# Performance work log

Hardware: AMD Instinct MI355X
Metric: run time of the kernel (lower is better)

## Reference

```python
import jax, jax.numpy as jnp
import numpy as np

N = 20000      # nodes
E = 160000     # edges (avg degree 16)
IN_DIM = 256
HID = 128      # hidden_dim == per-head out_channels in PyG TransformerConv
HEADS = 4
EPS = 1e-5


def setup_inputs() -> dict:
    key = jax.random.key(0)
    ks = jax.random.split(key, 24)

    def w(k, shape, scale=0.05):
        return jax.random.normal(k, shape, dtype=jnp.float32) * scale

    inp = {
        "x": jax.random.normal(ks[0], (N, IN_DIM), dtype=jnp.float32),
        "edge_index": jax.random.randint(ks[1], (2, E), 0, N, dtype=jnp.int32),
        # input projection
        "lin_w": w(ks[2], (IN_DIM, HID)), "lin_b": jnp.zeros((HID,), jnp.float32),
    }
    i = 3
    for l in (1, 2):
        inp[f"q_w{l}"] = w(ks[i], (HID, HEADS * HID)); i += 1
        inp[f"q_b{l}"] = jnp.zeros((HEADS * HID,), jnp.float32)
        inp[f"k_w{l}"] = w(ks[i], (HID, HEADS * HID)); i += 1
        inp[f"k_b{l}"] = jnp.zeros((HEADS * HID,), jnp.float32)
        inp[f"v_w{l}"] = w(ks[i], (HID, HEADS * HID)); i += 1
        inp[f"v_b{l}"] = jnp.zeros((HEADS * HID,), jnp.float32)
        inp[f"s_w{l}"] = w(ks[i], (HID, HID)); i += 1
        inp[f"s_b{l}"] = jnp.zeros((HID,), jnp.float32)
        inp[f"ln_g{l}"] = jnp.ones((HID,), jnp.float32)
        inp[f"ln_b{l}"] = jnp.zeros((HID,), jnp.float32)
    return inp


def _segment_softmax(scores, seg, num):
    # scores: [E, HEADS], seg: [E] destination indices
    m = jax.ops.segment_max(scores, seg, num_segments=num)
    m = jnp.where(jnp.isfinite(m), m, 0.0)  # guard empty segments
    e = jnp.exp(scores - m[seg])
    d = jax.ops.segment_sum(e, seg, num_segments=num)
    return e / (d[seg] + 1e-16)


def _transformer_conv(x, src, dst, qw, qb, kw, kb, vw, vb, sw, sb):
    # PyG TransformerConv(HID, HID, heads=HEADS, concat=False)
    n = x.shape[0]
    q = (x @ qw + qb).reshape(n, HEADS, HID)
    k = (x @ kw + kb).reshape(n, HEADS, HID)
    v = (x @ vw + vb).reshape(n, HEADS, HID)
    # per-edge attention: query at dst (i), key/value at src (j)
    alpha = jnp.einsum("ehd,ehd->eh", q[dst], k[src]) / jnp.sqrt(jnp.float32(HID))
    alpha = _segment_softmax(alpha, dst, n)                 # [E, HEADS]
    msg = v[src] * alpha[..., None]                          # [E, HEADS, HID]
    out = jax.ops.segment_sum(msg, dst, num_segments=n)      # [N, HEADS, HID]
    out = out.mean(axis=1)                                   # concat=False -> head mean
    return out + x @ sw + sb                                 # root skip connection


def _layer_norm(x, g, b):
    mu = x.mean(-1, keepdims=True)
    var = ((x - mu) ** 2).mean(-1, keepdims=True)
    return (x - mu) * jax.lax.rsqrt(var + EPS) * g + b


def reference(x, edge_index, lin_w, lin_b,
              q_w1, q_b1, k_w1, k_b1, v_w1, v_b1, s_w1, s_b1, ln_g1, ln_b1,
              q_w2, q_b2, k_w2, k_b2, v_w2, v_b2, s_w2, s_b2, ln_g2, ln_b2):
    src, dst = edge_index[0], edge_index[1]
    h = jax.nn.relu(x @ lin_w + lin_b)
    h1 = _transformer_conv(h, src, dst, q_w1, q_b1, k_w1, k_b1, v_w1, v_b1, s_w1, s_b1)
    h = _layer_norm(h1 + h, ln_g1, ln_b1)
    h2 = _transformer_conv(h, src, dst, q_w2, q_b2, k_w2, k_b2, v_w2, v_b2, s_w2, s_b2)
    h = _layer_norm(h2 + h, ln_g2, ln_b2)
    return h
```

## Files before the change

### kernel.cpp

```cpp
#include <hip/hip_runtime.h>
#include <math.h>

#define NNODE 20000
#define NEDGE 160000
#define IN_DIMV 256
#define HIDV 128
#define DEGCAP 64
#define BAT 4

typedef __attribute__((ext_vector_type(8))) short bf16x8;
typedef __attribute__((ext_vector_type(4))) float f32x4;
typedef __attribute__((ext_vector_type(2))) float f32x2;

__device__ __forceinline__ float bf2f(unsigned short u) {
    union { unsigned int i; float f; } x; x.i = ((unsigned int)u) << 16; return x.f;
}
__device__ __forceinline__ unsigned short f2bf(float f) {
    union { float f; unsigned int i; } x; x.f = f;
    unsigned int r = x.i + 0x7fffu + ((x.i >> 16) & 1u);
    return (unsigned short)(r >> 16);
}
__device__ __forceinline__ void unpack8(uint4 p, float* f) {
    f[0] = bf2f((unsigned short)(p.x & 0xffff)); f[1] = bf2f((unsigned short)(p.x >> 16));
    f[2] = bf2f((unsigned short)(p.y & 0xffff)); f[3] = bf2f((unsigned short)(p.y >> 16));
    f[4] = bf2f((unsigned short)(p.z & 0xffff)); f[5] = bf2f((unsigned short)(p.z >> 16));
    f[6] = bf2f((unsigned short)(p.w & 0xffff)); f[7] = bf2f((unsigned short)(p.w >> 16));
}
__device__ __forceinline__ void unpack8f8_w(unsigned int a, unsigned int b, float* f) {
    f32x2 t;
    t = __builtin_amdgcn_cvt_pk_f32_fp8((int)a, false); f[0] = t.x; f[1] = t.y;
    t = __builtin_amdgcn_cvt_pk_f32_fp8((int)a, true);  f[2] = t.x; f[3] = t.y;
    t = __builtin_amdgcn_cvt_pk_f32_fp8((int)b, false); f[4] = t.x; f[5] = t.y;
    t = __builtin_amdgcn_cvt_pk_f32_fp8((int)b, true);  f[6] = t.x; f[7] = t.y;
}
__device__ __forceinline__ unsigned char f2fp8(float v) {
    int pk = __builtin_amdgcn_cvt_pk_fp8_f32(v, v, 0, false);
    return (unsigned char)(pk & 0xff);
}
__device__ __forceinline__ void gld_lds16(const unsigned short* g, unsigned short* l) {
    __builtin_amdgcn_global_load_lds((const __attribute__((address_space(1))) void*)g,
                                     (__attribute__((address_space(3))) void*)l, 16, 0, 0);
}

__global__ void convert_kernel(
    const float* __restrict__ lin_w,
    const float* __restrict__ qw0, const float* __restrict__ kw0,
    const float* __restrict__ vw0, const float* __restrict__ sw0,
    const float* __restrict__ qw1, const float* __restrict__ kw1,
    const float* __restrict__ vw1, const float* __restrict__ sw1,
    unsigned short* __restrict__ arena, int* __restrict__ cursor)
{
    int idx = blockIdx.x * 256 + threadIdx.x;
    if (idx < NNODE) cursor[idx] = 0;
    int id2 = idx - NNODE;
    if (id2 < 0 || id2 >= 458752) return;
    float v;
    if (id2 < 32768) {
        int n = id2 >> 8, k = id2 & 255;
        v = lin_w[k * 128 + n];
    } else {
        int t = id2 - 32768;
        int l = t / 212992, r = t % 212992;
        int n = r >> 7, k = r & 127;
        const float* qw = l ? qw1 : qw0;
        const float* kw = l ? kw1 : kw0;
        const float* vw = l ? vw1 : vw0;
        const float* sw = l ? sw1 : sw0;
        if (n < 1536) {
            const float* w = (n < 512) ? qw : (n < 1024) ? kw : vw;
            v = w[k * 512 + (n & 511)];
        } else {
            v = sw[k * 128 + (n - 1536)];
        }
    }
    arena[id2] = f2bf(v);
}

__global__ __launch_bounds__(256) void mfma_gemm0(
    const float* __restrict__ A, const unsigned short* __restrict__ WT,
    const float* __restrict__ b0, unsigned short* __restrict__ hbf_out)
{
    __shared__ unsigned short smem[8192];
    unsigned short* As = smem;
    unsigned short* Bs = smem + 4096;
    unsigned short* ot = smem;
    const int K = 256;

    int tid = threadIdx.x;
    int lane = tid & 63;
    int w = tid >> 6;
    int wm = w & 1, wn = w >> 1;
    int bm = blockIdx.x * 128;

    int r0 = tid >> 2;
    int c0 = (tid & 3) * 8;
    int g0 = bm + r0;      if (g0 > NNODE - 1) g0 = NNODE - 1;
    int g1 = bm + r0 + 64; if (g1 > NNODE - 1) g1 = NNODE - 1;
    int srow = lane >> 2;
    int scol = (lane & 3) * 8;
    int br0 = w * 32 + srow;
    int br1 = w * 32 + 16 + srow;

    f32x4 acc[4][4] = {};
    int arow = wm * 64 + (lane & 15);
    int brow = wn * 64 + (lane & 15);
    int koff = (lane >> 4) * 8;

    for (int k0 = 0; k0 < K; k0 += 32) {
        {
            const float4* p0 = (const float4*)(A + (size_t)g0 * K + k0 + c0);
            float4 u = p0[0], v = p0[1];
            unsigned short t0[8] = {f2bf(u.x), f2bf(u.y), f2bf(u.z), f2bf(u.w),
                                    f2bf(v.x), f2bf(v.y), f2bf(v.z), f2bf(v.w)};
            *(uint4*)&As[r0 * 32 + c0] = *(uint4*)t0;
            const float4* p1 = (const float4*)(A + (size_t)g1 * K + k0 + c0);
            u = p1[0]; v = p1[1];
            unsigned short t1[8] = {f2bf(u.x), f2bf(u.y), f2bf(u.z), f2bf(u.w),
                                    f2bf(v.x), f2bf(v.y), f2bf(v.z), f2bf(v.w)};
            *(uint4*)&As[(r0 + 64) * 32 + c0] = *(uint4*)t1;
        }
        gld_lds16(WT + (size_t)br0 * K + k0 + scol, Bs + (w * 32) * 32);
        gld_lds16(WT + (size_t)br1 * K + k0 + scol, Bs + (w * 32 + 16) * 32);
        __syncthreads();
        bf16x8 fa[4], fb[4];
#pragma unroll
        for (int i = 0; i < 4; i++) fa[i] = *(const bf16x8*)&As[(arow + i * 16) * 32 + koff];
#pragma unroll
        for (int i = 0; i < 4; i++) fb[i] = *(const bf16x8*)&Bs[(brow + i * 16) * 32 + koff];
#pragma unroll
        for (int mi = 0; mi < 4; mi++)
#pragma unroll
            for (int ni = 0; ni < 4; ni++)
                acc[mi][ni] = __builtin_amdgcn_mfma_f32_16x16x32_bf16(fa[mi], fb[ni], acc[mi][ni], 0, 0, 0);
        __syncthreads();
    }

    int quad = lane >> 4, lcol = lane & 15;
#pragma unroll
    for (int hh = 0; hh < 2; hh++) {
        __syncthreads();
        if (wm == hh) {
#pragma unroll
            for (int mi = 0; mi < 4; mi++) {
#pragma unroll
                for (int ni = 0; ni < 4; ni++) {
                    int lc = wn * 64 + ni * 16 + lcol;
                    float bias = b0[lc];
#pragma unroll
                    for (int reg = 0; reg < 4; reg++) {
                        float v = fmaxf(acc[mi][ni][reg] + bias, 0.f);
                        ot[(mi * 16 + quad * 4 + reg) * 128 + lc] = f2bf(v);
                    }
                }
            }
        }
        __syncthreads();
        int r = tid >> 2, ch = tid & 3;
        int row = bm + hh * 64 + r;
        if (row < NNODE) {
            uint4* dp = (uint4*)(hbf_out + (size_t)row * HIDV + ch * 32);
            const uint4* sp = (const uint4*)(ot + r * 128 + ch * 32);
#pragma unroll
            for (int q = 0; q < 4; q++) dp[q] = sp[q];
        }
    }
}

__global__ __launch_bounds__(256) void mfma_gemm1(
    const unsigned short* __restrict__ A, const unsigned short* __restrict__ WT,
    const float* __restrict__ b0, const float* __restrict__ b1,
    const float* __restrict__ b2, const float* __restrict__ b3,
    unsigned short* __restrict__ qb_out, unsigned char* __restrict__ kv8_out,
    unsigned short* __restrict__ pre16_out)
{
    __shared__ unsigned short As[8192];
    __shared__ unsigned short Ws[16384];
    unsigned short* ot = Ws;
    unsigned char* ot8 = (unsigned char*)Ws;
    const int K = 128;

    int tid = threadIdx.x;
    int lane = tid & 63;
    int w = tid >> 6;
    int bm = blockIdx.x * 64;
    int p0 = (blockIdx.y == 0) ? 0 : 7;
    int p1 = (blockIdx.y == 0) ? 7 : 13;

    int srow = lane >> 2;
    int scol = (lane & 3) * 8;
    int asr = w * 16 + srow;
    int aar = bm + asr; if (aar > NNODE - 1) aar = NNODE - 1;
    int sr0 = w * 32 + srow;
    int sr1 = w * 32 + 16 + srow;

#pragma unroll
    for (int c = 0; c < 4; c++) {
        gld_lds16(A + (size_t)aar * K + c * 32 + scol, As + c * 2048 + asr * 32);
    }

    int arow = lane & 15;
    int koff = (lane >> 4) * 8;
    int quad = lane >> 4, lcol = lane & 15;

    for (int p = p0; p < p1; p++) {
        int bn = p * 128;
#pragma unroll
        for (int c = 0; c < 4; c++) {
            gld_lds16(WT + (size_t)(bn + sr0) * K + c * 32 + scol, Ws + c * 4096 + sr0 * 32);
            gld_lds16(WT + (size_t)(bn + sr1) * K + c * 32 + scol, Ws + c * 4096 + sr1 * 32);
        }
        __syncthreads();

        f32x4 acc[4][2] = {};
#pragma unroll
        for (int c = 0; c < 4; c++) {
            bf16x8 fa[4], fb[2];
#pragma unroll
            for (int i = 0; i < 4; i++) fa[i] = *(const bf16x8*)&As[c * 2048 + (arow + i * 16) * 32 + koff];
#pragma unroll
            for (int i = 0; i < 2; i++) fb[i] = *(const bf16x8*)&Ws[c * 4096 + (w * 32 + i * 16 + arow) * 32 + koff];
#pragma unroll
            for (int mi = 0; mi < 4; mi++)
#pragma unroll
                for (int ni = 0; ni < 2; ni++)
                    acc[mi][ni] = __builtin_amdgcn_mfma_f32_16x16x32_bf16(fa[mi], fb[ni], acc[mi][ni], 0, 0, 0);
        }
        __syncthreads();

        if (p < 4 || p == 12) {
            const float* bb = (p < 4) ? (b0 + bn) : b3;
#pragma unroll
            for (int mi = 0; mi < 4; mi++) {
#pragma unroll
                for (int ni = 0; ni < 2; ni++) {
                    int lc = w * 32 + ni * 16 + lcol;
                    float bias = bb[lc];
#pragma unroll
                    for (int reg = 0; reg < 4; reg++)
                        ot[(mi * 16 + quad * 4 + reg) * 128 + lc] = f2bf(acc[mi][ni][reg] + bias);
                }
            }
            __syncthreads();
            int r = tid >> 2, q = tid & 3;
            int row = bm + r;
            if (row < NNODE) {
                unsigned short* dst = (p < 4) ? (qb_out + (size_t)row * 512 + bn + q * 32)
                                              : (pre16_out + (size_t)row * HIDV + q * 32);
                const uint4* sp = (const uint4*)(ot + r * 128 + q * 32);
                uint4* dp = (uint4*)dst;
#pragma unroll
                for (int qq = 0; qq < 4; qq++) dp[qq] = sp[qq];
            }
            __syncthreads();
        } else {
            const float* bb = (bn < 1024) ? (b1 + bn - 512) : (b2 + bn - 1024);
            int coff = bn - 512;
#pragma unroll
            for (int mi = 0; mi < 4; mi++) {
#pragma unroll
                for (int ni = 0; ni < 2; ni++) {
                    int lc = w * 32 + ni * 16 + lcol;
                    float bias = bb[lc];
#pragma unroll
                    for (int reg = 0; reg < 4; reg++)
                        ot8[(mi * 16 + quad * 4 + reg) * 128 + lc] = f2fp8(acc[mi][ni][reg] + bias);
                }
            }
            __syncthreads();
            int r = tid >> 2, q = tid & 3;
            int row = bm + r;
            if (row < NNODE) {
                uint4* dp = (uint4*)(kv8_out + (size_t)row * 1024 + coff + q * 32);
                const uint4* sp = (const uint4*)(ot8 + r * 128 + q * 32);
                dp[0] = sp[0]; dp[1] = sp[1];
            }
            __syncthreads();
        }
    }
}

__global__ void scatter_kernel(const int* __restrict__ ei, int* __restrict__ cursor,
                               int* __restrict__ bucket) {
    int e = blockIdx.x * blockDim.x + threadIdx.x;
    if (e < NEDGE) {
        int d = ei[NEDGE + e];
        int slot = atomicAdd(&cursor[d], 1);
        if (slot < DEGCAP) bucket[d * DEGCAP + slot] = ei[e];
    }
}

__global__ __launch_bounds__(256) void attn_ln_kernel(
    const unsigned short* __restrict__ qb, const unsigned char* __restrict__ kv8,
    const int* __restrict__ cursor, const int* __restrict__ bucket,
    const unsigned short* __restrict__ pre16, const float* __restrict__ g,
    const float* __restrict__ b,
    unsigned short* __restrict__ hbf ,
    float* __restrict__ extout)
{
    int lane = threadIdx.x & 63;
    int wid = threadIdx.x >> 6;
    int i = blockIdx.x * 4 + wid;
    int myidx = bucket[i * DEGCAP + lane];
    int cnt = cursor[i]; if (cnt > DEGCAP) cnt = DEGCAP;

    int hg = lane >> 4;
    int sl = lane & 15;
    int off = hg * 128 + sl * 8;

    size_t base = (size_t)i * HIDV + sl * 8;
    uint4 pv_raw = *(const uint4*)(pre16 + base);
    uint4 hv_raw = *(const uint4*)(hbf + base);

    float qr[8];
    {
        uint4 p = *(const uint4*)(qb + (size_t)i * 512 + lane * 8);
        unpack8(p, qr);
#pragma unroll
        for (int j = 0; j < 8; j++) qr[j] *= 0.0883883476483184f;
    }

    float m = -INFINITY, l = 0.f;
    float acc[8] = {0.f, 0.f, 0.f, 0.f, 0.f, 0.f, 0.f, 0.f};

    if (cnt > 0) {
        uint2 kA[BAT], vA[BAT], kB[BAT], vB[BAT];

        auto issue = [&](uint2 (&KB)[BAT], uint2 (&VB)[BAT], int bb) {
#pragma unroll
            for (int t = 0; t < BAT; t++) {
                int j = bb * BAT + t; if (j >= cnt) j = cnt - 1;
                int src = __shfl(myidx, j);
                const unsigned char* bp = kv8 + (size_t)src * 1024 + off;
                KB[t] = *(const uint2*)bp;
                VB[t] = *(const uint2*)(bp + 512);
            }
        };

        auto consume = [&](const uint2 (&KB)[BAT], const uint2 (&VB)[BAT], int bb) {
            int rem = cnt - bb * BAT;
            float d[BAT];
#pragma unroll
            for (int t = 0; t < BAT; t++) d[t] = -3.0e38f;
#pragma unroll
            for (int t = 0; t < BAT; t++) {
                if (t >= rem) break;
                float kf[8];
                unpack8f8_w(KB[t].x, KB[t].y, kf);
                d[t] = qr[0] * kf[0] + qr[1] * kf[1] + qr[2] * kf[2] + qr[3] * kf[3] +
                       qr[4] * kf[4] + qr[5] * kf[5] + qr[6] * kf[6] + qr[7] * kf[7];
            }
#pragma unroll
            for (int t = 0; t < BAT; t++) { if (t >= rem) break; d[t] += __shfl_xor(d[t], 8); }
#pragma unroll
            for (int t = 0; t < BAT; t++) { if (t >= rem) break; d[t] += __shfl_xor(d[t], 4); }
#pragma unroll
            for (int t = 0; t < BAT; t++) { if (t >= rem) break; d[t] += __shfl_xor(d[t], 2); }
#pragma unroll
            for (int t = 0; t < BAT; t++) { if (t >= rem) break; d[t] += __shfl_xor(d[t], 1); }

            float mq = d[0];
#pragma unroll
            for (int t = 1; t < BAT; t++) mq = fmaxf(mq, d[t]);
            float mn = fmaxf(m, mq);
            float scale = __expf(m - mn);
            float p[BAT];
            float psum = 0.f;
#pragma unroll
            for (int t = 0; t < BAT; t++) { p[t] = __expf(d[t] - mn); psum += p[t]; }
            l = l * scale + psum;
            m = mn;
#pragma unroll
            for (int c = 0; c < 8; c++) acc[c] *= scale;
#pragma unroll
            for (int t = 0; t < BAT; t++) {
                if (t >= rem) break;
                float vf[8];
                unpack8f8_w(VB[t].x, VB[t].y, vf);
                float pt = p[t];
#pragma unroll
                for (int c = 0; c < 8; c++) acc[c] += pt * vf[c];
            }
        };

        int nb = (cnt + BAT - 1) >> 2;
        issue(kA, vA, 0);
        for (int bb = 0; bb < nb; bb += 2) {
            if (bb + 1 < nb) issue(kB, vB, bb + 1);
            consume(kA, vA, bb);
            if (bb + 1 < nb) {
                if (bb + 2 < nb) issue(kA, vA, bb + 2);
                consume(kB, vB, bb + 1);
            }
        }
    }

    float linv = 0.25f / (l + 1e-16f);
#pragma unroll
    for (int c = 0; c < 8; c++) acc[c] *= linv;
#pragma unroll
    for (int c = 0; c < 8; c++) {
        acc[c] += __shfl_xor(acc[c], 16);
        acc[c] += __shfl_xor(acc[c], 32);
    }

    float pv[8], hv[8];
    unpack8(pv_raw, pv);
    unpack8(hv_raw, hv);
    float vals[8];
#pragma unroll
    for (int c = 0; c < 8; c++) vals[c] = acc[c] + pv[c] + hv[c];

    float s = 0.f;
#pragma unroll
    for (int c = 0; c < 8; c++) s += vals[c];
    s += __shfl_xor(s, 1); s += __shfl_xor(s, 2);
    s += __shfl_xor(s, 4); s += __shfl_xor(s, 8);
    float mu = s * (1.f / 128.f);
    float vs = 0.f;
#pragma unroll
    for (int c = 0; c < 8; c++) { float dx = vals[c] - mu; vs += dx * dx; }
    vs += __shfl_xor(vs, 1); vs += __shfl_xor(vs, 2);
    vs += __shfl_xor(vs, 4); vs += __shfl_xor(vs, 8);
    float rstd = rsqrtf(vs * (1.f / 128.f) + 1e-5f);

    float4 g0 = ((const float4*)(g + sl * 8))[0];
    float4 g1 = ((const float4*)(g + sl * 8))[1];
    float4 bb0 = ((const float4*)(b + sl * 8))[0];
    float4 bb1 = ((const float4*)(b + sl * 8))[1];
    float y[8];
    y[0] = (vals[0] - mu) * rstd * g0.x + bb0.x; y[1] = (vals[1] - mu) * rstd * g0.y + bb0.y;
    y[2] = (vals[2] - mu) * rstd * g0.z + bb0.z; y[3] = (vals[3] - mu) * rstd * g0.w + bb0.w;
    y[4] = (vals[4] - mu) * rstd * g1.x + bb1.x; y[5] = (vals[5] - mu) * rstd * g1.y + bb1.y;
    y[6] = (vals[6] - mu) * rstd * g1.z + bb1.z; y[7] = (vals[7] - mu) * rstd * g1.w + bb1.w;

    if (lane < 16) {
        unsigned short tmp[8] = {f2bf(y[0]), f2bf(y[1]), f2bf(y[2]), f2bf(y[3]),
                                 f2bf(y[4]), f2bf(y[5]), f2bf(y[6]), f2bf(y[7])};
        *(uint4*)(hbf + base) = *(uint4*)tmp;
        if (extout) {
            ((float4*)(extout + base))[0] = make_float4(y[0], y[1], y[2], y[3]);
            ((float4*)(extout + base))[1] = make_float4(y[4], y[5], y[6], y[7]);
        }
    }
}

extern "C" void kernel_launch(void* const* d_in, const int* in_sizes, int n_in,
                              void* d_out, int out_size, void* d_ws, size_t ws_size,
                              hipStream_t stream) {
    const float* x = (const float*)d_in[0];
    const int* ei = (const int*)d_in[1];

    char* ws = (char*)d_ws;
    unsigned short* hbf = (unsigned short*)(ws + 0);
    unsigned short* pre16 = (unsigned short*)(ws + 5120000);
    unsigned short* qb = (unsigned short*)(ws + 10240000);
    unsigned char* kv8 = (unsigned char*)(ws + 30720000);
    int* cursor = (int*)(ws + 51200000);
    int* bucket = (int*)(ws + 51280000);
    unsigned short* arena = (unsigned short*)(ws + 56400000);

    convert_kernel<<<(NNODE + 458752 + 255) / 256, 256, 0, stream>>>(
        (const float*)d_in[2],
        (const float*)d_in[4], (const float*)d_in[6], (const float*)d_in[8], (const float*)d_in[10],
        (const float*)d_in[14], (const float*)d_in[16], (const float*)d_in[18], (const float*)d_in[20],
        arena, cursor);

    scatter_kernel<<<(NEDGE + 255) / 256, 256, 0, stream>>>(ei, cursor, bucket);

    const int GM = (NNODE + 127) / 128;
    const int GM64 = (NNODE + 63) / 64;

    mfma_gemm0<<<GM, 256, 0, stream>>>(x, arena, (const float*)d_in[3], hbf);

    for (int l = 0; l < 2; l++) {
        int o = 4 + l * 10;
        const unsigned short* WT = arena + 32768 + l * 212992;
        mfma_gemm1<<<dim3(GM64, 2), 256, 0, stream>>>(
            hbf, WT,
            (const float*)d_in[o + 1], (const float*)d_in[o + 3],
            (const float*)d_in[o + 5], (const float*)d_in[o + 7],
            qb, kv8, pre16);

        attn_ln_kernel<<<NNODE / 4, 256, 0, stream>>>(
            qb, kv8, cursor, bucket, pre16,
            (const float*)d_in[o + 8], (const float*)d_in[o + 9],
            hbf, (l == 1) ? (float*)d_out : nullptr);
    }
}
```

Measured before the change: 271.9 us.

## Make attention kernel persistent with grid-stride nodes and prefetch of next node

The attention+layernorm kernel now launches a fixed grid of 1024 blocks (4096 waves). Each wave loops over nodes with a stride of 4096 and prefetches the next node's bucket indices, degree, query, pre-activation and hidden row while it processes the current node. The aim is to hide the per-node header load latency and amortise the gamma/beta loads and launch overhead. It adds register pressure, with launch_bounds raised to request 4 blocks per SM, and fewer waves in flight may reduce latency hiding on the gather loads.

```diff
diff --git a/kernel.cpp b/kernel.cpp
--- a/kernel.cpp
+++ b/kernel.cpp
@@ -289,7 +289,8 @@
     }
 }
 
-__global__ __launch_bounds__(256) void attn_ln_kernel(
+#define AGW 4096
+__global__ __launch_bounds__(256, 4) void attn_ln_kernel(
     const unsigned short* __restrict__ qb, const unsigned char* __restrict__ kv8,
     const int* __restrict__ cursor, const int* __restrict__ bucket,
     const unsigned short* __restrict__ pre16, const float* __restrict__ g,
@@ -299,148 +300,170 @@
 {
     int lane = threadIdx.x & 63;
     int wid = threadIdx.x >> 6;
-    int i = blockIdx.x * 4 + wid;
-    int myidx = bucket[i * DEGCAP + lane];
-    int cnt = cursor[i]; if (cnt > DEGCAP) cnt = DEGCAP;
+    int gw = blockIdx.x * 4 + wid;
 
     int hg = lane >> 4;
     int sl = lane & 15;
     int off = hg * 128 + sl * 8;
 
-    size_t base = (size_t)i * HIDV + sl * 8;
-    uint4 pv_raw = *(const uint4*)(pre16 + base);
-    uint4 hv_raw = *(const uint4*)(hbf + base);
-
-    float qr[8];
-    {
-        uint4 p = *(const uint4*)(qb + (size_t)i * 512 + lane * 8);
-        unpack8(p, qr);
-#pragma unroll
-        for (int j = 0; j < 8; j++) qr[j] *= 0.0883883476483184f;
-    }
-
-    float m = -INFINITY, l = 0.f;
-    float acc[8] = {0.f, 0.f, 0.f, 0.f, 0.f, 0.f, 0.f, 0.f};
-
-    if (cnt > 0) {
-        uint2 kA[BAT], vA[BAT], kB[BAT], vB[BAT];
-
-        auto issue = [&](uint2 (&KB)[BAT], uint2 (&VB)[BAT], int bb) {
-#pragma unroll
-            for (int t = 0; t < BAT; t++) {
-                int j = bb * BAT + t; if (j >= cnt) j = cnt - 1;
-                int src = __shfl(myidx, j);
-                const unsigned char* bp = kv8 + (size_t)src * 1024 + off;
-                KB[t] = *(const uint2*)bp;
-                VB[t] = *(const uint2*)(bp + 512);
-            }
-        };
-
-        auto consume = [&](const uint2 (&KB)[BAT], const uint2 (&VB)[BAT], int bb) {
-            int rem = cnt - bb * BAT;
-            float d[BAT];
-#pragma unroll
-            for (int t = 0; t < BAT; t++) d[t] = -3.0e38f;
-#pragma unroll
-            for (int t = 0; t < BAT; t++) {
-                if (t >= rem) break;
-                float kf[8];
-                unpack8f8_w(KB[t].x, KB[t].y, kf);
-                d[t] = qr[0] * kf[0] + qr[1] * kf[1] + qr[2] * kf[2] + qr[3] * kf[3] +
-                       qr[4] * kf[4] + qr[5] * kf[5] + qr[6] * kf[6] + qr[7] * kf[7];
-            }
-#pragma unroll
-            for (int t = 0; t < BAT; t++) { if (t >= rem) break; d[t] += __shfl_xor(d[t], 8); }
-#pragma unroll
-            for (int t = 0; t < BAT; t++) { if (t >= rem) break; d[t] += __shfl_xor(d[t], 4); }
-#pragma unroll
-            for (int t = 0; t < BAT; t++) { if (t >= rem) break; d[t] += __shfl_xor(d[t], 2); }
-#pragma unroll
-            for (int t = 0; t < BAT; t++) { if (t >= rem) break; d[t] += __shfl_xor(d[t], 1); }
-
-            float mq = d[0];
-#pragma unroll
-            for (int t = 1; t < BAT; t++) mq = fmaxf(mq, d[t]);
-            float mn = fmaxf(m, mq);
-            float scale = __expf(m - mn);
-            float p[BAT];
-            float psum = 0.f;
-#pragma unroll
-            for (int t = 0; t < BAT; t++) { p[t] = __expf(d[t] - mn); psum += p[t]; }
-            l = l * scale + psum;
-            m = mn;
-#pragma unroll
-            for (int c = 0; c < 8; c++) acc[c] *= scale;
-#pragma unroll
-            for (int t = 0; t < BAT; t++) {
-                if (t >= rem) break;
-                float vf[8];
-                unpack8f8_w(VB[t].x, VB[t].y, vf);
-                float pt = p[t];
-#pragma unroll
-                for (int c = 0; c < 8; c++) acc[c] += pt * vf[c];
-            }
-        };
-
-        int nb = (cnt + BAT - 1) >> 2;
-        issue(kA, vA, 0);
-        for (int bb = 0; bb < nb; bb += 2) {
-            if (bb + 1 < nb) issue(kB, vB, bb + 1);
-            consume(kA, vA, bb);
-            if (bb + 1 < nb) {
-                if (bb + 2 < nb) issue(kA, vA, bb + 2);
-                consume(kB, vB, bb + 1);
-            }
-        }
-    }
-
-    float linv = 0.25f / (l + 1e-16f);
-#pragma unroll
-    for (int c = 0; c < 8; c++) acc[c] *= linv;
-#pragma unroll
-    for (int c = 0; c < 8; c++) {
-        acc[c] += __shfl_xor(acc[c], 16);
-        acc[c] += __shfl_xor(acc[c], 32);
-    }
-
-    float pv[8], hv[8];
-    unpack8(pv_raw, pv);
-    unpack8(hv_raw, hv);
-    float vals[8];
-#pragma unroll
-    for (int c = 0; c < 8; c++) vals[c] = acc[c] + pv[c] + hv[c];
-
-    float s = 0.f;
-#pragma unroll
-    for (int c = 0; c < 8; c++) s += vals[c];
-    s += __shfl_xor(s, 1); s += __shfl_xor(s, 2);
-    s += __shfl_xor(s, 4); s += __shfl_xor(s, 8);
-    float mu = s * (1.f / 128.f);
-    float vs = 0.f;
-#pragma unroll
-    for (int c = 0; c < 8; c++) { float dx = vals[c] - mu; vs += dx * dx; }
-    vs += __shfl_xor(vs, 1); vs += __shfl_xor(vs, 2);
-    vs += __shfl_xor(vs, 4); vs += __shfl_xor(vs, 8);
-    float rstd = rsqrtf(vs * (1.f / 128.f) + 1e-5f);
-
     float4 g0 = ((const float4*)(g + sl * 8))[0];
     float4 g1 = ((const float4*)(g + sl * 8))[1];
-    float4 bb0 = ((const float4*)(b + sl * 8))[0];
-    float4 bb1 = ((const float4*)(b + sl * 8))[1];
-    float y[8];
-    y[0] = (vals[0] - mu) * rstd * g0.x + bb0.x; y[1] = (vals[1] - mu) * rstd * g0.y + bb0.y;
-    y[2] = (vals[2] - mu) * rstd * g0.z + bb0.z; y[3] = (vals[3] - mu) * rstd * g0.w + bb0.w;
-    y[4] = (vals[4] - mu) * rstd * g1.x + bb1.x; y[5] = (vals[5] - mu) * rstd * g1.y + bb1.y;
-    y[6] = (vals[6] - mu) * rstd * g1.z + bb1.z; y[7] = (vals[7] - mu) * rstd * g1.w + bb1.w;
-
-    if (lane < 16) {
-        unsigned short tmp[8] = {f2bf(y[0]), f2bf(y[1]), f2bf(y[2]), f2bf(y[3]),
-                                 f2bf(y[4]), f2bf(y[5]), f2bf(y[6]), f2bf(y[7])};
-        *(uint4*)(hbf + base) = *(uint4*)tmp;
-        if (extout) {
-            ((float4*)(extout + base))[0] = make_float4(y[0], y[1], y[2], y[3]);
-            ((float4*)(extout + base))[1] = make_float4(y[4], y[5], y[6], y[7]);
-        }
+    float4 bg0 = ((const float4*)(b + sl * 8))[0];
+    float4 bg1 = ((const float4*)(b + sl * 8))[1];
+
+    int cidx, ccnt;
+    uint4 cq, cpv, chv;
+    {
+        int i = gw;
+        cidx = bucket[i * DEGCAP + lane];
+        ccnt = cursor[i];
+        cq = *(const uint4*)(qb + (size_t)i * 512 + lane * 8);
+        cpv = *(const uint4*)(pre16 + (size_t)i * HIDV + sl * 8);
+        chv = *(const uint4*)(hbf + (size_t)i * HIDV + sl * 8);
+    }
+
+    for (int i = gw; i < NNODE; i += AGW) {
+        int inext = i + AGW;
+        int nidx = 0, ncnt = 0;
+        uint4 nq = {}, npv = {}, nhv = {};
+        if (inext < NNODE) {
+            nidx = bucket[inext * DEGCAP + lane];
+            ncnt = cursor[inext];
+            nq = *(const uint4*)(qb + (size_t)inext * 512 + lane * 8);
+            npv = *(const uint4*)(pre16 + (size_t)inext * HIDV + sl * 8);
+            nhv = *(const uint4*)(hbf + (size_t)inext * HIDV + sl * 8);
+        }
+
+        int cnt = ccnt; if (cnt > DEGCAP) cnt = DEGCAP;
+        int myidx = cidx;
+
+        float qr[8];
+        unpack8(cq, qr);
+#pragma unroll
+        for (int j = 0; j < 8; j++) qr[j] *= 0.0883883476483184f;
+
+        float m = -INFINITY, l = 0.f;
+        float acc[8] = {0.f, 0.f, 0.f, 0.f, 0.f, 0.f, 0.f, 0.f};
+
+        if (cnt > 0) {
+            uint2 kA[BAT], vA[BAT], kB[BAT], vB[BAT];
+
+            auto issue = [&](uint2 (&KB)[BAT], uint2 (&VB)[BAT], int bb) {
+#pragma unroll
+                for (int t = 0; t < BAT; t++) {
+                    int j = bb * BAT + t; if (j >= cnt) j = cnt - 1;
+                    int src = __shfl(myidx, j);
+                    const unsigned char* bp = kv8 + (size_t)src * 1024 + off;
+                    KB[t] = *(const uint2*)bp;
+                    VB[t] = *(const uint2*)(bp + 512);
+                }
+            };
+
+            auto consume = [&](const uint2 (&KB)[BAT], const uint2 (&VB)[BAT], int bb) {
+                int rem = cnt - bb * BAT;
+                float d[BAT];
+#pragma unroll
+                for (int t = 0; t < BAT; t++) d[t] = -3.0e38f;
+#pragma unroll
+                for (int t = 0; t < BAT; t++) {
+                    if (t >= rem) break;
+                    float kf[8];
+                    unpack8f8_w(KB[t].x, KB[t].y, kf);
+                    d[t] = qr[0] * kf[0] + qr[1] * kf[1] + qr[2] * kf[2] + qr[3] * kf[3] +
+                           qr[4] * kf[4] + qr[5] * kf[5] + qr[6] * kf[6] + qr[7] * kf[7];
+                }
+#pragma unroll
+                for (int t = 0; t < BAT; t++) { if (t >= rem) break; d[t] += __shfl_xor(d[t], 8); }
+#pragma unroll
+                for (int t = 0; t < BAT; t++) { if (t >= rem) break; d[t] += __shfl_xor(d[t], 4); }
+#pragma unroll
+                for (int t = 0; t < BAT; t++) { if (t >= rem) break; d[t] += __shfl_xor(d[t], 2); }
+#pragma unroll
+                for (int t = 0; t < BAT; t++) { if (t >= rem) break; d[t] += __shfl_xor(d[t], 1); }
+
+                float mq = d[0];
+#pragma unroll
+                for (int t = 1; t < BAT; t++) mq = fmaxf(mq, d[t]);
+                float mn = fmaxf(m, mq);
+                float scale = __expf(m - mn);
+                float p[BAT];
+                float psum = 0.f;
+#pragma unroll
+                for (int t = 0; t < BAT; t++) { p[t] = __expf(d[t] - mn); psum += p[t]; }
+                l = l * scale + psum;
+                m = mn;
+#pragma unroll
+                for (int c = 0; c < 8; c++) acc[c] *= scale;
+#pragma unroll
+                for (int t = 0; t < BAT; t++) {
+                    if (t >= rem) break;
+                    float vf[8];
+                    unpack8f8_w(VB[t].x, VB[t].y, vf);
+                    float pt = p[t];
+#pragma unroll
+                    for (int c = 0; c < 8; c++) acc[c] += pt * vf[c];
+                }
+            };
+
+            int nb = (cnt + BAT - 1) >> 2;
+            issue(kA, vA, 0);
+            for (int bb = 0; bb < nb; bb += 2) {
+                if (bb + 1 < nb) issue(kB, vB, bb + 1);
+                consume(kA, vA, bb);
+                if (bb + 1 < nb) {
+                    if (bb + 2 < nb) issue(kA, vA, bb + 2);
+                    consume(kB, vB, bb + 1);
+                }
+            }
+        }
+
+        float linv = 0.25f / (l + 1e-16f);
+#pragma unroll
+        for (int c = 0; c < 8; c++) acc[c] *= linv;
+#pragma unroll
+        for (int c = 0; c < 8; c++) {
+            acc[c] += __shfl_xor(acc[c], 16);
+            acc[c] += __shfl_xor(acc[c], 32);
+        }
+
+        float pv[8], hv[8];
+        unpack8(cpv, pv);
+        unpack8(chv, hv);
+        float vals[8];
+#pragma unroll
+        for (int c = 0; c < 8; c++) vals[c] = acc[c] + pv[c] + hv[c];
+
+        float s = 0.f;
+#pragma unroll
+        for (int c = 0; c < 8; c++) s += vals[c];
+        s += __shfl_xor(s, 1); s += __shfl_xor(s, 2);
+        s += __shfl_xor(s, 4); s += __shfl_xor(s, 8);
+        float mu = s * (1.f / 128.f);
+        float vs = 0.f;
+#pragma unroll
+        for (int c = 0; c < 8; c++) { float dx = vals[c] - mu; vs += dx * dx; }
+        vs += __shfl_xor(vs, 1); vs += __shfl_xor(vs, 2);
+        vs += __shfl_xor(vs, 4); vs += __shfl_xor(vs, 8);
+        float rstd = rsqrtf(vs * (1.f / 128.f) + 1e-5f);
+
+        float y[8];
+        y[0] = (vals[0] - mu) * rstd * g0.x + bg0.x; y[1] = (vals[1] - mu) * rstd * g0.y + bg0.y;
+        y[2] = (vals[2] - mu) * rstd * g0.z + bg0.z; y[3] = (vals[3] - mu) * rstd * g0.w + bg0.w;
+        y[4] = (vals[4] - mu) * rstd * g1.x + bg1.x; y[5] = (vals[5] - mu) * rstd * g1.y + bg1.y;
+        y[6] = (vals[6] - mu) * rstd * g1.z + bg1.z; y[7] = (vals[7] - mu) * rstd * g1.w + bg1.w;
+
+        size_t base = (size_t)i * HIDV + sl * 8;
+        if (lane < 16) {
+            unsigned short tmp[8] = {f2bf(y[0]), f2bf(y[1]), f2bf(y[2]), f2bf(y[3]),
+                                     f2bf(y[4]), f2bf(y[5]), f2bf(y[6]), f2bf(y[7])};
+            *(uint4*)(hbf + base) = *(uint4*)tmp;
+            if (extout) {
+                ((float4*)(extout + base))[0] = make_float4(y[0], y[1], y[2], y[3]);
+                ((float4*)(extout + base))[1] = make_float4(y[4], y[5], y[6], y[7]);
+            }
+        }
+
+        cidx = nidx; ccnt = ncnt; cq = nq; cpv = npv; chv = nhv;
     }
 }
 
@@ -481,7 +504,7 @@
             (const float*)d_in[o + 5], (const float*)d_in[o + 7],
             qb, kv8, pre16);
 
-        attn_ln_kernel<<<NNODE / 4, 256, 0, stream>>>(
+        attn_ln_kernel<<<1024, 256, 0, stream>>>(
             qb, kv8, cursor, bucket, pre16,
             (const float*)d_in[o + 8], (const float*)d_in[o + 9],
             hbf, (l == 1) ? (float*)d_out : nullptr);
```

Measured after the change: 273.2 us. Within noise of the previous version (+0.5%).
